# Kernel tuning notes

Hardware: AMD Instinct MI355X
Metric: run time of the kernel (lower is better)

## Reference

```python
import jax, jax.numpy as jnp
import numpy as np

OUT, IN, R = 8192, 8192, 16
GROUP = 16
SCALING = 16.0 / 16.0  # lora_alpha / r
# nvfp4 (e2m1) code table: 3 low bits magnitude, bit 3 = sign
NVFP4_LUT = jnp.array([0.0, 0.5, 1.0, 1.5, 2.0, 3.0, 4.0, 6.0,
                       -0.0, -0.5, -1.0, -1.5, -2.0, -3.0, -4.0, -6.0],
                      dtype=jnp.float32)


def setup_inputs() -> dict:
    key = jax.random.key(0)
    k1, k2, k3, k4, k5 = jax.random.split(key, 5)
    x = jax.random.normal(k1, (64, IN), dtype=jnp.float32)
    packed_weight = jax.random.randint(k2, (OUT, IN // 2), 0, 256, dtype=jnp.int32).astype(jnp.uint8)
    # effective block scales (global scale already absorbed, as in _load_prequantized_nvfp4)
    weight_block_scales = (jax.random.uniform(k3, (OUT, IN // GROUP), dtype=jnp.float32) + 0.1) * 0.01
    lora_A = jax.random.normal(k4, (R, IN), dtype=jnp.float32) * (1.0 / np.sqrt(IN))
    lora_B = jax.random.normal(k5, (OUT, R), dtype=jnp.float32) * 0.01
    return {"x": x, "packed_weight": packed_weight,
            "weight_block_scales": weight_block_scales,
            "lora_A": lora_A, "lora_B": lora_B}


def _dequant_nvfp4(packed, block_scales):
    # packed: (OUT, IN//2) uint8, two fp4 codes per byte (low nibble = even index)
    low = (packed & 0xF).astype(jnp.int32)
    high = (packed >> 4).astype(jnp.int32)
    codes = jnp.stack([low, high], axis=-1).reshape(packed.shape[0], -1)  # (OUT, IN)
    vals = NVFP4_LUT[codes]
    O, I = vals.shape
    # per-block scale over groups of GROUP along in_features
    W = (vals.reshape(O, I // GROUP, GROUP) * block_scales[:, :, None]).reshape(O, I)
    return W


def reference(x, packed_weight, weight_block_scales, lora_A, lora_B):
    W = _dequant_nvfp4(packed_weight, weight_block_scales)      # (OUT, IN) fp32
    base = x @ W.T                                              # (B, OUT)
    lora = (x @ lora_A.T) @ lora_B.T                            # (B, OUT)
    return base + SCALING * lora
```

## Files before the change

kernel.cpp:

```cpp
#include <hip/hip_runtime.h>
#include <stdint.h>

#define IN_F   8192
#define OUT_F  8192
#define MB     64
#define RANK   16

typedef _Float16 f16x8 __attribute__((ext_vector_type(8)));
typedef _Float16 f16x2 __attribute__((ext_vector_type(2)));
typedef float    f32x4 __attribute__((ext_vector_type(4)));

__device__ __forceinline__ unsigned pk2h(float a, float b) {
    return __builtin_bit_cast(unsigned, __builtin_amdgcn_cvt_pkrtz(a, b));
}

__device__ __forceinline__ f16x8 decode8(unsigned p, unsigned s2) {
    unsigned q  = p >> 4;
    unsigned me = __builtin_amdgcn_perm(0x46444240u, 0x3E3C3800u, p & 0x07070707u);
    unsigned mo = __builtin_amdgcn_perm(0x46444240u, 0x3E3C3800u, q & 0x07070707u);
    unsigned he = ((p & 0x08080808u) << 4) | me;
    unsigned ho = ((q & 0x08080808u) << 4) | mo;
    unsigned bu0 = __builtin_amdgcn_perm(ho, he, 0x040C000Cu);
    unsigned bu1 = __builtin_amdgcn_perm(ho, he, 0x050C010Cu);
    unsigned bu2 = __builtin_amdgcn_perm(ho, he, 0x060C020Cu);
    unsigned bu3 = __builtin_amdgcn_perm(ho, he, 0x070C030Cu);
    f16x2 sv = __builtin_bit_cast(f16x2, s2);
    f16x2 h0 = __builtin_bit_cast(f16x2, bu0) * sv;
    f16x2 h1 = __builtin_bit_cast(f16x2, bu1) * sv;
    f16x2 h2 = __builtin_bit_cast(f16x2, bu2) * sv;
    f16x2 h3 = __builtin_bit_cast(f16x2, bu3) * sv;
    f16x8 b;
    b[0]=h0[0]; b[1]=h0[1]; b[2]=h1[0]; b[3]=h1[1];
    b[4]=h2[0]; b[5]=h2[1]; b[6]=h3[0]; b[7]=h3[1];
    return b;
}

__global__ void detect_kernel(const unsigned* __restrict__ Wp,
                              int* __restrict__ flag, float* __restrict__ t) {
    unsigned v = Wp[threadIdx.x & 63];
    unsigned long long m = __ballot(v > 255u);
    if (threadIdx.x == 0) *flag = (m == 0ull) ? 1 : 0;
    for (int i = threadIdx.x; i < MB * RANK; i += 256) t[i] = 0.f;
}

__global__ __launch_bounds__(256) void prep_kernel(
    const float* __restrict__ x, const float* __restrict__ lora_A,
    uint2* __restrict__ xf2, float* __restrict__ t)
{
    const int m = blockIdx.x, kq = blockIdx.y;
    const int tid = threadIdx.x;
    const int mt = m >> 4, l15 = m & 15;
    float acc[RANK];
#pragma unroll
    for (int r = 0; r < RANK; ++r) acc[r] = 0.f;

    const float4* x4 = (const float4*)(x + (size_t)m * IN_F);
    const float4* A4 = (const float4*)lora_A;
#pragma unroll
    for (int it = 0; it < 2; ++it) {
        int j = kq * 512 + it * 256 + tid;
        float4 xv = x4[j];
        uint2 u;
        u.x = pk2h(xv.x, xv.y);
        u.y = pk2h(xv.z, xv.w);
        int kstep = j >> 3, quad = (j >> 1) & 3, h = j & 1;
        xf2[(size_t)(((kstep * 4 + mt) * 64 + quad * 16 + l15) * 2 + h)] = u;
#pragma unroll
        for (int r = 0; r < RANK; ++r) {
            float4 av = A4[(size_t)r * (IN_F / 4) + j];
            acc[r] += xv.x * av.x + xv.y * av.y + xv.z * av.z + xv.w * av.w;
        }
    }
#pragma unroll
    for (int r = 0; r < RANK; ++r)
#pragma unroll
        for (int off = 32; off > 0; off >>= 1)
            acc[r] += __shfl_down(acc[r], off);

    __shared__ float red[4][RANK];
    int lane = tid & 63, wid = tid >> 6;
    if (lane == 0) {
#pragma unroll
        for (int r = 0; r < RANK; ++r) red[wid][r] = acc[r];
    }
    __syncthreads();
    if (tid < RANK)
        atomicAdd(&t[m * RANK + tid],
                  red[0][tid] + red[1][tid] + red[2][tid] + red[3][tid]);
}

__global__ __launch_bounds__(256) void lora_kernel(
    const float* __restrict__ t, const float* __restrict__ lora_B,
    float* __restrict__ out)
{
    const int gid = blockIdx.x * 256 + threadIdx.x;
    const int m = gid >> 11;
    const int n4 = (gid & 2047) * 4;
    const float4* t4 = (const float4*)(t + m * RANK);
    float4 ta = t4[0], tb = t4[1], tc = t4[2], td = t4[3];
    float4 o;
    float* op = (float*)&o;
#pragma unroll
    for (int j = 0; j < 4; ++j) {
        const float4* B4 = (const float4*)(lora_B + (size_t)(n4 + j) * RANK);
        float4 b0 = B4[0], b1 = B4[1], b2 = B4[2], b3 = B4[3];
        op[j] = ta.x * b0.x + ta.y * b0.y + ta.z * b0.z + ta.w * b0.w
              + tb.x * b1.x + tb.y * b1.y + tb.z * b1.z + tb.w * b1.w
              + tc.x * b2.x + tc.y * b2.y + tc.z * b2.z + tc.w * b2.w
              + td.x * b3.x + td.y * b3.y + td.z * b3.z + td.w * b3.w;
    }
    ((float4*)out)[gid] = o;
}

template<int FMT>
__global__ __launch_bounds__(1024, 4) void main_kernel(
    const void*  __restrict__ Wpv,
    const float* __restrict__ scales,
    const uint4* __restrict__ xf4,
    const int*   __restrict__ flag,
    float*       __restrict__ out)
{
    if (*flag != FMT) return;

    __shared__ float lds[16 * 1024];

    const int tid = threadIdx.x;
    const int lane = tid & 63, w = tid >> 6;
    const int l15 = lane & 15, quad = lane >> 4;
    const int n0 = blockIdx.x * 16;
    const int row = n0 + l15;

    f32x4 acc[4];
#pragma unroll
    for (int mt = 0; mt < 4; ++mt) acc[mt] = (f32x4){0.f, 0.f, 0.f, 0.f};

    const uint4*    wi = (const uint4*)Wpv + (size_t)row * (IN_F / 8) + w * 64 + quad;
    const unsigned* wb = (const unsigned*)((const uint8_t*)Wpv
                         + (size_t)row * (IN_F / 2)) + w * 64 + quad;
    const float*    sp = scales + (size_t)row * (IN_F / 16) + w * 32 + (quad >> 1);

#pragma unroll 4
    for (int s = 0; s < 16; ++s) {
        const int kstep = w * 16 + s;
        f16x8 afr[4];
#pragma unroll
        for (int mt = 0; mt < 4; ++mt)
            afr[mt] = __builtin_bit_cast(f16x8, xf4[(size_t)(kstep * 4 + mt) * 64 + lane]);

        unsigned p;
        if (FMT == 1) {
            uint4 v = wi[s * 4];
            p = v.x | (v.y << 8) | (v.z << 16) | (v.w << 24);
        } else {
            p = wb[s * 4];
        }
        float sc = sp[s * 2];
        unsigned s2 = pk2h(sc, sc);
        f16x8 b = decode8(p, s2);
#pragma unroll
        for (int mt = 0; mt < 4; ++mt)
            acc[mt] = __builtin_amdgcn_mfma_f32_16x16x32_f16(afr[mt], b, acc[mt], 0, 0, 0);
    }

#pragma unroll
    for (int mt = 0; mt < 4; ++mt)
#pragma unroll
        for (int r = 0; r < 4; ++r)
            lds[w * 1024 + (mt * 16 + quad * 4 + r) * 16 + l15] = acc[mt][r];
    __syncthreads();

    float sum = 0.f;
#pragma unroll
    for (int w2 = 0; w2 < 16; ++w2) sum += lds[w2 * 1024 + tid];
    const int m = tid >> 4, nl = tid & 15;
    const size_t idx = (size_t)m * OUT_F + n0 + nl;
    out[idx] += sum;
}

extern "C" void kernel_launch(void* const* d_in, const int* in_sizes, int n_in,
                              void* d_out, int out_size, void* d_ws, size_t ws_size,
                              hipStream_t stream)
{
    (void)in_sizes; (void)n_in; (void)out_size; (void)ws_size;
    const float* x      = (const float*)d_in[0];
    const void*  Wp     = (const void*)d_in[1];
    const float* scales = (const float*)d_in[2];
    const float* lora_A = (const float*)d_in[3];
    const float* lora_B = (const float*)d_in[4];
    float* out = (float*)d_out;

    char* ws = (char*)d_ws;
    int*   flag = (int*)ws;
    float* t    = (float*)(ws + 4096);
    uint2* xf   = (uint2*)(ws + 65536);

    detect_kernel<<<1, 256, 0, stream>>>((const unsigned*)Wp, flag, t);
    prep_kernel<<<dim3(64, 4), 256, 0, stream>>>(x, lora_A, xf, t);
    lora_kernel<<<512, 256, 0, stream>>>(t, lora_B, out);
    main_kernel<1><<<OUT_F / 16, 1024, 0, stream>>>(
        Wp, scales, (const uint4*)xf, flag, out);
    main_kernel<0><<<OUT_F / 16, 1024, 0, stream>>>(
        Wp, scales, (const uint4*)xf, flag, out);
}
```

Before: 258.4 us.

## Halve block size and software-pipeline weight and activation loads in main kernel

The main GEMV-like kernel now uses 512 threads per block, with each wave covering twice as many k-steps (32 instead of 16). Weight, scale and activation fragments are double-buffered in registers so the next chunk's loads are issued before the current chunk's MFMAs. Scales are loaded as float4 vectors instead of scalars. The aim is to hide global-load latency and shrink the cross-wave LDS reduction, at the cost of more registers per thread and less wave-level parallelism per block.

```diff
diff --git a/kernel.cpp b/kernel.cpp
--- a/kernel.cpp
+++ b/kernel.cpp
@@ -113,7 +113,7 @@
 }
 
 template<int FMT>
-__global__ __launch_bounds__(1024, 4) void main_kernel(
+__global__ __launch_bounds__(512, 4) void main_kernel(
     const void*  __restrict__ Wpv,
     const float* __restrict__ scales,
     const uint4* __restrict__ xf4,
@@ -122,11 +122,11 @@
 {
     if (*flag != FMT) return;
 
-    __shared__ float lds[16 * 1024];
+    __shared__ float lds[8 * 1024];
 
     const int tid = threadIdx.x;
     const int lane = tid & 63, w = tid >> 6;
-    const int l15 = lane & 15, quad = lane >> 4;
+    const int l15 = lane & 15, quad = lane >> 4, qh = quad >> 1;
     const int n0 = blockIdx.x * 16;
     const int row = n0 + l15;
 
@@ -134,33 +134,82 @@
 #pragma unroll
     for (int mt = 0; mt < 4; ++mt) acc[mt] = (f32x4){0.f, 0.f, 0.f, 0.f};
 
-    const uint4*    wi = (const uint4*)Wpv + (size_t)row * (IN_F / 8) + w * 64 + quad;
-    const unsigned* wb = (const unsigned*)((const uint8_t*)Wpv
-                         + (size_t)row * (IN_F / 2)) + w * 64 + quad;
-    const float*    sp = scales + (size_t)row * (IN_F / 16) + w * 32 + (quad >> 1);
-
-#pragma unroll 4
-    for (int s = 0; s < 16; ++s) {
-        const int kstep = w * 16 + s;
-        f16x8 afr[4];
-#pragma unroll
-        for (int mt = 0; mt < 4; ++mt)
-            afr[mt] = __builtin_bit_cast(f16x8, xf4[(size_t)(kstep * 4 + mt) * 64 + lane]);
-
-        unsigned p;
-        if (FMT == 1) {
-            uint4 v = wi[s * 4];
-            p = v.x | (v.y << 8) | (v.z << 16) | (v.w << 24);
+    const uint4*    wi  = (const uint4*)Wpv + (size_t)row * (IN_F / 8) + w * 128 + quad;
+    const unsigned* wb  = (const unsigned*)Wpv + (size_t)row * (IN_F / 8) + w * 128 + quad;
+    const float4*   sp4 = (const float4*)(scales + (size_t)row * (IN_F / 16)) + w * 16;
+    const uint4*    xfp = xf4 + (size_t)(w * 32 * 4) * 64 + lane;
+
+    uint4 wvA[4], wvB[4];
+    unsigned wpA[4], wpB[4];
+    float4 scA[2], scB[2];
+    uint4 xvA[4], xvB[4];
+
+#define LOADW(c, wv, wp, sc)                                             \
+    do {                                                                 \
+        if (FMT == 1) {                                                  \
+            wv[0] = wi[(c)*16];     wv[1] = wi[(c)*16 + 4];              \
+            wv[2] = wi[(c)*16 + 8]; wv[3] = wi[(c)*16 + 12];             \
+        } else {                                                         \
+            wp[0] = wb[(c)*16];     wp[1] = wb[(c)*16 + 4];              \
+            wp[2] = wb[(c)*16 + 8]; wp[3] = wb[(c)*16 + 12];             \
+        }                                                                \
+        sc[0] = sp4[(c)*2]; sc[1] = sp4[(c)*2 + 1];                      \
+    } while (0)
+
+#define LOADX(s, xv)                                                     \
+    do {                                                                 \
+        xv[0] = xfp[(size_t)((s)*4 + 0) * 64];                           \
+        xv[1] = xfp[(size_t)((s)*4 + 1) * 64];                           \
+        xv[2] = xfp[(size_t)((s)*4 + 2) * 64];                           \
+        xv[3] = xfp[(size_t)((s)*4 + 3) * 64];                           \
+    } while (0)
+
+#define STEPC(wv, wp, st, scf4, xv)                                      \
+    do {                                                                 \
+        unsigned p;                                                      \
+        if (FMT == 1) {                                                  \
+            uint4 v = wv[st];                                            \
+            p = v.x | (v.y << 8) | (v.z << 16) | (v.w << 24);            \
+        } else p = wp[st];                                               \
+        float scf = ((st) & 1) ? (qh ? scf4[(st) >> 1].w : scf4[(st) >> 1].z) \
+                               : (qh ? scf4[(st) >> 1].y : scf4[(st) >> 1].x); \
+        unsigned s2 = pk2h(scf, scf);                                    \
+        f16x8 b = decode8(p, s2);                                        \
+        acc[0] = __builtin_amdgcn_mfma_f32_16x16x32_f16(                 \
+            __builtin_bit_cast(f16x8, xv[0]), b, acc[0], 0, 0, 0);       \
+        acc[1] = __builtin_amdgcn_mfma_f32_16x16x32_f16(                 \
+            __builtin_bit_cast(f16x8, xv[1]), b, acc[1], 0, 0, 0);       \
+        acc[2] = __builtin_amdgcn_mfma_f32_16x16x32_f16(                 \
+            __builtin_bit_cast(f16x8, xv[2]), b, acc[2], 0, 0, 0);       \
+        acc[3] = __builtin_amdgcn_mfma_f32_16x16x32_f16(                 \
+            __builtin_bit_cast(f16x8, xv[3]), b, acc[3], 0, 0, 0);       \
+    } while (0)
+
+    LOADW(0, wvA, wpA, scA);
+    LOADX(0, xvA);
+
+#pragma unroll
+    for (int c = 0; c < 8; ++c) {
+        const int s0 = c * 4;
+        if ((c & 1) == 0) {
+            if (c < 7) LOADW(c + 1, wvB, wpB, scB);
+            LOADX(s0 + 1, xvB);  STEPC(wvA, wpA, 0, scA, xvA);
+            LOADX(s0 + 2, xvA);  STEPC(wvA, wpA, 1, scA, xvB);
+            LOADX(s0 + 3, xvB);  STEPC(wvA, wpA, 2, scA, xvA);
+            if (s0 + 4 < 32) LOADX(s0 + 4, xvA);
+            STEPC(wvA, wpA, 3, scA, xvB);
         } else {
-            p = wb[s * 4];
+            if (c < 7) LOADW(c + 1, wvA, wpA, scA);
+            LOADX(s0 + 1, xvB);  STEPC(wvB, wpB, 0, scB, xvA);
+            LOADX(s0 + 2, xvA);  STEPC(wvB, wpB, 1, scB, xvB);
+            LOADX(s0 + 3, xvB);  STEPC(wvB, wpB, 2, scB, xvA);
+            if (s0 + 4 < 32) LOADX(s0 + 4, xvA);
+            STEPC(wvB, wpB, 3, scB, xvB);
         }
-        float sc = sp[s * 2];
-        unsigned s2 = pk2h(sc, sc);
-        f16x8 b = decode8(p, s2);
-#pragma unroll
-        for (int mt = 0; mt < 4; ++mt)
-            acc[mt] = __builtin_amdgcn_mfma_f32_16x16x32_f16(afr[mt], b, acc[mt], 0, 0, 0);
-    }
+    }
+#undef LOADW
+#undef LOADX
+#undef STEPC
 
 #pragma unroll
     for (int mt = 0; mt < 4; ++mt)
@@ -169,12 +218,15 @@
             lds[w * 1024 + (mt * 16 + quad * 4 + r) * 16 + l15] = acc[mt][r];
     __syncthreads();
 
-    float sum = 0.f;
-#pragma unroll
-    for (int w2 = 0; w2 < 16; ++w2) sum += lds[w2 * 1024 + tid];
-    const int m = tid >> 4, nl = tid & 15;
-    const size_t idx = (size_t)m * OUT_F + n0 + nl;
-    out[idx] += sum;
+    float s0 = 0.f, s1 = 0.f;
+#pragma unroll
+    for (int w2 = 0; w2 < 8; ++w2) {
+        s0 += lds[w2 * 1024 + tid];
+        s1 += lds[w2 * 1024 + 512 + tid];
+    }
+    const int m0 = tid >> 4, nl = tid & 15;
+    out[(size_t)m0 * OUT_F + n0 + nl] += s0;
+    out[(size_t)(m0 + 32) * OUT_F + n0 + nl] += s1;
 }
 
 extern "C" void kernel_launch(void* const* d_in, const int* in_sizes, int n_in,
@@ -197,8 +249,8 @@
     detect_kernel<<<1, 256, 0, stream>>>((const unsigned*)Wp, flag, t);
     prep_kernel<<<dim3(64, 4), 256, 0, stream>>>(x, lora_A, xf, t);
     lora_kernel<<<512, 256, 0, stream>>>(t, lora_B, out);
-    main_kernel<1><<<OUT_F / 16, 1024, 0, stream>>>(
+    main_kernel<1><<<OUT_F / 16, 512, 0, stream>>>(
         Wp, scales, (const uint4*)xf, flag, out);
-    main_kernel<0><<<OUT_F / 16, 1024, 0, stream>>>(
+    main_kernel<0><<<OUT_F / 16, 512, 0, stream>>>(
         Wp, scales, (const uint4*)xf, flag, out);
 }
```

Measured after the change: 252.5 us. 2.3% less time.

## Split-K main GEMM with LDS-staged activations and partial-sum reduction kernel

Applied to the files above, without the earlier changes.

Restructures the dequant-GEMM so each block owns one K-slice and 256 output rows. The block stages its activation slice in LDS once and reuses it across 8 waves, each handling two 16-row tiles. Weights and scales are prefetched with double-buffered register loads, and a separate finish kernel reduces the 16 partial buffers and fuses in the LoRA term. When the workspace is small it falls back to atomic accumulation into the output. The aim is to cut redundant activation reads and the per-block LDS reduction, at the cost of 32 MB of partial traffic or atomics.

```diff
diff --git a/kernel.cpp b/kernel.cpp
--- a/kernel.cpp
+++ b/kernel.cpp
@@ -5,6 +5,8 @@
 #define OUT_F  8192
 #define MB     64
 #define RANK   16
+#define KSPLIT 16
+#define KSTEPS 16
 
 typedef _Float16 f16x8 __attribute__((ext_vector_type(8)));
 typedef _Float16 f16x2 __attribute__((ext_vector_type(2)));
@@ -89,13 +91,8 @@
                   red[0][tid] + red[1][tid] + red[2][tid] + red[3][tid]);
 }
 
-__global__ __launch_bounds__(256) void lora_kernel(
-    const float* __restrict__ t, const float* __restrict__ lora_B,
-    float* __restrict__ out)
-{
-    const int gid = blockIdx.x * 256 + threadIdx.x;
-    const int m = gid >> 11;
-    const int n4 = (gid & 2047) * 4;
+__device__ __forceinline__ float4 lora4(const float* __restrict__ t, int m,
+                                        const float* __restrict__ lora_B, int n4) {
     const float4* t4 = (const float4*)(t + m * RANK);
     float4 ta = t4[0], tb = t4[1], tc = t4[2], td = t4[3];
     float4 o;
@@ -109,79 +106,160 @@
               + tc.x * b2.x + tc.y * b2.y + tc.z * b2.z + tc.w * b2.w
               + td.x * b3.x + td.y * b3.y + td.z * b3.z + td.w * b3.w;
     }
-    ((float4*)out)[gid] = o;
-}
-
-template<int FMT>
-__global__ __launch_bounds__(1024, 4) void main_kernel(
+    return o;
+}
+
+__global__ __launch_bounds__(256) void lora_kernel(
+    const float* __restrict__ t, const float* __restrict__ lora_B,
+    float* __restrict__ out)
+{
+    const int gid = blockIdx.x * 256 + threadIdx.x;
+    ((float4*)out)[gid] = lora4(t, gid >> 11, lora_B, (gid & 2047) * 4);
+}
+
+__global__ __launch_bounds__(256) void finish_kernel(
+    const float* __restrict__ partial, const float* __restrict__ t,
+    const float* __restrict__ lora_B, float* __restrict__ out)
+{
+    const int gid = blockIdx.x * 256 + threadIdx.x;
+    float4 p = {0.f, 0.f, 0.f, 0.f};
+#pragma unroll
+    for (int ksp = 0; ksp < KSPLIT; ++ksp) {
+        float4 v = ((const float4*)partial)[(size_t)ksp * (MB * OUT_F / 4) + gid];
+        p.x += v.x; p.y += v.y; p.z += v.z; p.w += v.w;
+    }
+    float4 l = lora4(t, gid >> 11, lora_B, (gid & 2047) * 4);
+    p.x += l.x; p.y += l.y; p.z += l.z; p.w += l.w;
+    ((float4*)out)[gid] = p;
+}
+
+template<int FMT, int ATOMIC>
+__global__ __launch_bounds__(512, 4) void main_kernel(
     const void*  __restrict__ Wpv,
     const float* __restrict__ scales,
     const uint4* __restrict__ xf4,
     const int*   __restrict__ flag,
-    float*       __restrict__ out)
+    float*       __restrict__ dst)
 {
     if (*flag != FMT) return;
 
-    __shared__ float lds[16 * 1024];
+    __shared__ __align__(16) char xs[65536];
 
     const int tid = threadIdx.x;
     const int lane = tid & 63, w = tid >> 6;
-    const int l15 = lane & 15, quad = lane >> 4;
-    const int n0 = blockIdx.x * 16;
+    const int l15 = lane & 15, quad = lane >> 4, qh = quad >> 1;
+    const int ks = blockIdx.x;
+    const int n0 = blockIdx.y * 256 + w * 32;
     const int row = n0 + l15;
 
-    f32x4 acc[4];
-#pragma unroll
-    for (int mt = 0; mt < 4; ++mt) acc[mt] = (f32x4){0.f, 0.f, 0.f, 0.f};
-
-    const uint4*    wi = (const uint4*)Wpv + (size_t)row * (IN_F / 8) + w * 64 + quad;
-    const unsigned* wb = (const unsigned*)((const uint8_t*)Wpv
-                         + (size_t)row * (IN_F / 2)) + w * 64 + quad;
-    const float*    sp = scales + (size_t)row * (IN_F / 16) + w * 32 + (quad >> 1);
-
-#pragma unroll 4
-    for (int s = 0; s < 16; ++s) {
-        const int kstep = w * 16 + s;
-        f16x8 afr[4];
+    {
+        const uint4* gsrc = xf4 + (size_t)ks * (KSTEPS * 4 * 64);
+#pragma unroll
+        for (int i = 0; i < 8; ++i) {
+            int idx = i * 512 + tid;
+            uint4 v = gsrc[idx];
+            *(uint4*)&xs[(size_t)idx * 16] = v;
+        }
+    }
+    __syncthreads();
+
+    f32x4 acc[4][2];
+#pragma unroll
+    for (int mt = 0; mt < 4; ++mt)
+#pragma unroll
+        for (int nt = 0; nt < 2; ++nt)
+            acc[mt][nt] = (f32x4){0.f, 0.f, 0.f, 0.f};
+
+    const uint4*    wi0 = (const uint4*)Wpv + (size_t)row * (IN_F / 8) + ks * 64 + quad;
+    const uint4*    wi1 = wi0 + (size_t)16 * (IN_F / 8);
+    const unsigned* wb0 = (const unsigned*)Wpv + (size_t)row * (IN_F / 8) + ks * 64 + quad;
+    const unsigned* wb1 = wb0 + (size_t)16 * (IN_F / 8);
+    const float4*   sp4 = (const float4*)(scales + (size_t)row * (IN_F / 16) + ks * 32);
+    const float4*   sq4 = (const float4*)(scales + (size_t)(row + 16) * (IN_F / 16) + ks * 32);
+
+    uint4    wv[2][2][4];
+    unsigned wp[2][2][4];
+    float4   sc[2][2][2];
+
+#define LOADCH(buf, c)                                                   \
+    do {                                                                 \
+        _Pragma("unroll")                                                \
+        for (int j = 0; j < 4; ++j) {                                    \
+            if (FMT == 1) {                                              \
+                wv[buf][0][j] = wi0[((c) * 4 + j) * 4];                  \
+                wv[buf][1][j] = wi1[((c) * 4 + j) * 4];                  \
+            } else {                                                     \
+                wp[buf][0][j] = wb0[((c) * 4 + j) * 4];                  \
+                wp[buf][1][j] = wb1[((c) * 4 + j) * 4];                  \
+            }                                                            \
+        }                                                                \
+        sc[buf][0][0] = sp4[(c) * 2]; sc[buf][0][1] = sp4[(c) * 2 + 1];  \
+        sc[buf][1][0] = sq4[(c) * 2]; sc[buf][1][1] = sq4[(c) * 2 + 1];  \
+    } while (0)
+
+    LOADCH(0, 0);
+    LOADCH(1, 1);
+
+#pragma unroll
+    for (int c = 0; c < 4; ++c) {
+        const int buf = c & 1;
+#pragma unroll
+        for (int j = 0; j < 4; ++j) {
+            const int s = c * 4 + j;
+            f16x8 afr[4];
+#pragma unroll
+            for (int mt = 0; mt < 4; ++mt)
+                afr[mt] = *(const f16x8*)&xs[(size_t)(((s * 4 + mt) * 64) + lane) * 16];
+#pragma unroll
+            for (int nt = 0; nt < 2; ++nt) {
+                float4 v = sc[buf][nt][j >> 1];
+                float scf = (j & 1) ? (qh ? v.w : v.z) : (qh ? v.y : v.x);
+                unsigned s2 = pk2h(scf, scf);
+                unsigned p;
+                if (FMT == 1) {
+                    uint4 u = wv[buf][nt][j];
+                    p = u.x | (u.y << 8) | (u.z << 16) | (u.w << 24);
+                } else {
+                    p = wp[buf][nt][j];
+                }
+                f16x8 b = decode8(p, s2);
+#pragma unroll
+                for (int mt = 0; mt < 4; ++mt)
+                    acc[mt][nt] = __builtin_amdgcn_mfma_f32_16x16x32_f16(
+                        afr[mt], b, acc[mt][nt], 0, 0, 0);
+            }
+        }
+        if (c < 2) LOADCH(buf, c + 2);
+    }
+#undef LOADCH
+
+    if (ATOMIC == 0) {
+        float* pb = dst + (size_t)ks * (MB * OUT_F);
 #pragma unroll
         for (int mt = 0; mt < 4; ++mt)
-            afr[mt] = __builtin_bit_cast(f16x8, xf4[(size_t)(kstep * 4 + mt) * 64 + lane]);
-
-        unsigned p;
-        if (FMT == 1) {
-            uint4 v = wi[s * 4];
-            p = v.x | (v.y << 8) | (v.z << 16) | (v.w << 24);
-        } else {
-            p = wb[s * 4];
-        }
-        float sc = sp[s * 2];
-        unsigned s2 = pk2h(sc, sc);
-        f16x8 b = decode8(p, s2);
+#pragma unroll
+            for (int nt = 0; nt < 2; ++nt)
+#pragma unroll
+                for (int r = 0; r < 4; ++r)
+                    pb[(size_t)(mt * 16 + quad * 4 + r) * OUT_F + n0 + nt * 16 + l15]
+                        = acc[mt][nt][r];
+    } else {
 #pragma unroll
         for (int mt = 0; mt < 4; ++mt)
-            acc[mt] = __builtin_amdgcn_mfma_f32_16x16x32_f16(afr[mt], b, acc[mt], 0, 0, 0);
-    }
-
-#pragma unroll
-    for (int mt = 0; mt < 4; ++mt)
-#pragma unroll
-        for (int r = 0; r < 4; ++r)
-            lds[w * 1024 + (mt * 16 + quad * 4 + r) * 16 + l15] = acc[mt][r];
-    __syncthreads();
-
-    float sum = 0.f;
-#pragma unroll
-    for (int w2 = 0; w2 < 16; ++w2) sum += lds[w2 * 1024 + tid];
-    const int m = tid >> 4, nl = tid & 15;
-    const size_t idx = (size_t)m * OUT_F + n0 + nl;
-    out[idx] += sum;
+#pragma unroll
+            for (int nt = 0; nt < 2; ++nt)
+#pragma unroll
+                for (int r = 0; r < 4; ++r)
+                    atomicAdd(&dst[(size_t)(mt * 16 + quad * 4 + r) * OUT_F
+                                   + n0 + nt * 16 + l15], acc[mt][nt][r]);
+    }
 }
 
 extern "C" void kernel_launch(void* const* d_in, const int* in_sizes, int n_in,
                               void* d_out, int out_size, void* d_ws, size_t ws_size,
                               hipStream_t stream)
 {
-    (void)in_sizes; (void)n_in; (void)out_size; (void)ws_size;
+    (void)in_sizes; (void)n_in; (void)out_size;
     const float* x      = (const float*)d_in[0];
     const void*  Wp     = (const void*)d_in[1];
     const float* scales = (const float*)d_in[2];
@@ -190,15 +268,28 @@
     float* out = (float*)d_out;
 
     char* ws = (char*)d_ws;
-    int*   flag = (int*)ws;
-    float* t    = (float*)(ws + 4096);
-    uint2* xf   = (uint2*)(ws + 65536);
+    int*   flag    = (int*)ws;
+    float* t       = (float*)(ws + 4096);
+    uint2* xf      = (uint2*)(ws + 65536);
+    float* partial = (float*)(ws + (2u << 20));
+
+    const bool big_ws = ws_size >= ((size_t)34 << 20);
 
     detect_kernel<<<1, 256, 0, stream>>>((const unsigned*)Wp, flag, t);
     prep_kernel<<<dim3(64, 4), 256, 0, stream>>>(x, lora_A, xf, t);
-    lora_kernel<<<512, 256, 0, stream>>>(t, lora_B, out);
-    main_kernel<1><<<OUT_F / 16, 1024, 0, stream>>>(
-        Wp, scales, (const uint4*)xf, flag, out);
-    main_kernel<0><<<OUT_F / 16, 1024, 0, stream>>>(
-        Wp, scales, (const uint4*)xf, flag, out);
-}
+
+    if (big_ws) {
+        main_kernel<1, 0><<<dim3(KSPLIT, 32), 512, 0, stream>>>(
+            Wp, scales, (const uint4*)xf, flag, partial);
+        main_kernel<0, 0><<<dim3(KSPLIT, 32), 512, 0, stream>>>(
+            Wp, scales, (const uint4*)xf, flag, partial);
+        finish_kernel<<<(MB * OUT_F / 4) / 256, 256, 0, stream>>>(
+            partial, t, lora_B, out);
+    } else {
+        lora_kernel<<<(MB * OUT_F / 4) / 256, 256, 0, stream>>>(t, lora_B, out);
+        main_kernel<1, 1><<<dim3(KSPLIT, 32), 512, 0, stream>>>(
+            Wp, scales, (const uint4*)xf, flag, out);
+        main_kernel<0, 1><<<dim3(KSPLIT, 32), 512, 0, stream>>>(
+            Wp, scales, (const uint4*)xf, flag, out);
+    }
+}
```

Result: faster. 246.6 us (-4.6%).
